# Performance work log

Measured on AMD Instinct MI355X. Metric: run time of the kernel, lower is better.

The kernel has to match this reference:

```python
import jax, jax.numpy as jnp
import numpy as np

B, D, H = 4096, 66, 512  # batch, system dim (22 atoms * 3), MLP hidden


def _dynamics(t, xs, W1, b1, W2, b2, W3, b3):
    # CNF vector field f(t, x): 3-layer SiLU MLP on concat([x, t])
    h = jnp.concatenate([xs, t], axis=1)          # [B, D+1]
    h = jax.nn.silu(h @ W1 + b1)                  # [B, H]
    h = jax.nn.silu(h @ W2 + b2)                  # [B, H]
    return h @ W3 + b3                            # [B, D]


def setup_inputs() -> dict:
    key = jax.random.key(0)
    ks = jax.random.split(key, 5)
    xs = jax.random.normal(ks[0], (B, D), dtype=jnp.float32)
    t = jax.random.uniform(ks[1], (B, 1), dtype=jnp.float32)
    W1 = jax.random.normal(ks[2], (D + 1, H), dtype=jnp.float32) / np.float32(np.sqrt(D + 1))
    b1 = jnp.zeros((H,), dtype=jnp.float32)
    W2 = jax.random.normal(ks[3], (H, H), dtype=jnp.float32) / np.float32(np.sqrt(H))
    b2 = jnp.zeros((H,), dtype=jnp.float32)
    W3 = jax.random.normal(ks[4], (H, D), dtype=jnp.float32) / np.float32(np.sqrt(H))
    b3 = jnp.zeros((D,), dtype=jnp.float32)
    return {"xs": xs, "t": t, "W1": W1, "b1": b1, "W2": W2, "b2": b2, "W3": W3, "b3": b3}


def reference(xs, t, W1, b1, W2, b2, W3, b3):
    # Exact divergence: trace of Jacobian d f / d x, computed with D JVPs
    # (forward-mode equivalent of the torch per-dim autograd.grad loop).
    def f(x):
        return _dynamics(t, x, W1, b1, W2, b2, W3, b3)

    dxs = f(xs)                                   # [B, D]
    eye = jnp.eye(D, dtype=xs.dtype)              # basis vectors e_i

    def jvp_col(e):
        _, tang = jax.jvp(f, (xs,), (jnp.broadcast_to(e, xs.shape),))
        return tang                               # J @ e_i, shape [B, D]

    tangs = jax.vmap(jvp_col)(eye)                # [D, B, D]
    div = jnp.einsum('dbd->b', tangs)             # sum_i (J e_i)_i = tr(J)
    return dxs, -div[:, None]
```

## Files before the change

### kernel.cpp

```cpp
#include <hip/hip_runtime.h>

#define Bn 4096
#define Dn 66
#define Hn 512

typedef __attribute__((ext_vector_type(8))) short short8;
typedef __attribute__((ext_vector_type(4))) float f32x4;

__device__ __forceinline__ unsigned short f2bf(float x) {
    union { float f; unsigned u; } v; v.f = x;
    unsigned r = v.u + 0x7fffu + ((v.u >> 16) & 1u);
    return (unsigned short)(r >> 16);
}
__device__ __forceinline__ float bf2f(unsigned short h) {
    union { float f; unsigned u; } v; v.u = ((unsigned)h) << 16; return v.f;
}


__global__ __launch_bounds__(512, 2) void k_pack(
    const float* __restrict__ W1, const float* __restrict__ W2,
    const float* __restrict__ W3,
    unsigned short* __restrict__ WQ, unsigned short* __restrict__ W3P)
{
    __shared__ float sW3[16*68];
    const int bid = blockIdx.x, tid = threadIdx.x;
    const int lane = tid & 63, wv = tid >> 6;

    if (bid < 64) {
        const int ct = bid >> 1;
        {
            const int r = tid >> 5, ii = tid & 31;
            const float* src = &W3[(size_t)(ct*16 + r)*Dn];
            sW3[r*68 + ii] = src[ii];
            sW3[r*68 + ii + 32] = src[ii + 32];
            if (ii < 2) sW3[r*68 + ii + 64] = src[ii + 64];
        }
        __syncthreads();
        const int ks = (bid & 1)*8 + wv;
        const int n = lane & 15, kg = lane >> 4;
        const int c = ct*16 + n;
        const int abase = ks*32 + kg*8;
        float w2v[8], m[8];
        #pragma unroll
        for (int j = 0; j < 8; ++j) {
            w2v[j] = W2[(size_t)(abase + j)*Hn + c];
            m[j] = 0.f;
        }
        #pragma unroll 2
        for (int i = 0; i < Dn; ++i) {
            const float w3 = sW3[n*68 + i];
            const float4 w1a = *(const float4*)&W1[(size_t)i*Hn + abase];
            const float4 w1b = *(const float4*)&W1[(size_t)i*Hn + abase + 4];
            m[0] = fmaf(w3, w1a.x, m[0]); m[1] = fmaf(w3, w1a.y, m[1]);
            m[2] = fmaf(w3, w1a.z, m[2]); m[3] = fmaf(w3, w1a.w, m[3]);
            m[4] = fmaf(w3, w1b.x, m[4]); m[5] = fmaf(w3, w1b.y, m[5]);
            m[6] = fmaf(w3, w1b.z, m[6]); m[7] = fmaf(w3, w1b.w, m[7]);
        }
        short8 pw, pc;
        #pragma unroll
        for (int j = 0; j < 8; ++j) {
            pw[j] = (short)f2bf(w2v[j]);
            pc[j] = (short)f2bf(w2v[j] * m[j]);
        }
        const size_t off = ((size_t)(ct*16 + ks)*64 + lane)*16;
        *(short8*)&WQ[off]     = pw;
        *(short8*)&WQ[off + 8] = pc;
    } else {
        const int tix = (bid - 64)*8 + wv;
        if (tix < 80) {
            const int ks = tix & 15;
            const int n = lane & 15, kg = lane >> 4;
            const int j_out = (tix >> 4)*16 + n;
            const int abase = ks*32 + kg*8;
            short8 p;
            #pragma unroll
            for (int j = 0; j < 8; ++j)
                p[j] = (j_out < Dn) ? (short)f2bf(W3[(size_t)(abase + j)*Dn + j_out]) : (short)0;
            *(short8*)&W3P[((size_t)tix*64 + lane)*8] = p;
        }
    }
}

__global__ __launch_bounds__(1024, 4) void k_main(
    const float* __restrict__ xs, const float* __restrict__ tt,
    const float* __restrict__ W1, const float* __restrict__ b1,
    const unsigned short* __restrict__ WQ, const float* __restrict__ b2,
    const unsigned short* __restrict__ W3P, const float* __restrict__ b3,
    float* __restrict__ out)
{
    __shared__ __align__(16) unsigned short sA[2*8192];
    __shared__ float sX[67*16];
    __shared__ float sRed[16*16];

    const int tid = threadIdx.x, lane = tid & 63, wv = tid >> 6;
    const int rt = blockIdx.x, r0 = rt*16;
    const int n = lane & 15, kg = lane >> 4;
    const int rot = (blockIdx.x >> 3) & 15;

    for (int idx = tid; idx < 67*16; idx += 1024) {
        const int i = idx >> 4, r = idx & 15;
        sX[idx] = (i < Dn) ? xs[(size_t)(r0+r)*Dn + i] : tt[r0+r];
    }
    __syncthreads();

    {
        const int rg = lane & 7, cg = lane >> 3;
        const int c0 = wv*32 + cg*4;
        const int irot = (blockIdx.x >> 3) & 31;
        float z[2][4];
        {
            const float4 b4 = *(const float4*)&b1[c0];
            z[0][0]=b4.x; z[0][1]=b4.y; z[0][2]=b4.z; z[0][3]=b4.w;
            z[1][0]=b4.x; z[1][1]=b4.y; z[1][2]=b4.z; z[1][3]=b4.w;
        }
        #pragma unroll 2
        for (int s = 0; s < 67; ++s) {
            int i = s + irot; if (i >= 67) i -= 67;
            const float2 xf = *(const float2*)&sX[i*16 + 2*rg];
            const float4 wA = *(const float4*)&W1[(size_t)i*Hn + c0];
            const float ww[4] = {wA.x, wA.y, wA.z, wA.w};
            #pragma unroll
            for (int j = 0; j < 4; ++j) {
                z[0][j] = fmaf(xf.x, ww[j], z[0][j]);
                z[1][j] = fmaf(xf.y, ww[j], z[1][j]);
            }
        }
        const int kgrp = cg >> 1, joff = (cg & 1)*4;
        #pragma unroll
        for (int rr = 0; rr < 2; ++rr) {
            const int r = 2*(lane & 7) + rr;
            ushort4 phi, ps;
            unsigned short* PH = (unsigned short*)&phi;
            unsigned short* PS = (unsigned short*)&ps;
            #pragma unroll
            for (int j = 0; j < 4; ++j) {
                const float zv = z[rr][j];
                const float sg = 1.f / (1.f + __expf(-zv));
                PH[j] = f2bf(zv * sg);
                PS[j] = f2bf(sg * (1.f + zv * (1.f - sg)));
            }
            const int off = (wv*64 + r + 16*kgrp)*8 + joff;
            *(ushort4*)&sA[off]        = phi;
            *(ushort4*)&sA[8192 + off] = ps;
        }
    }
    __syncthreads();

    const int ctb = wv*2;
    f32x4 zac[2], vac[2];
    #pragma unroll
    for (int ti = 0; ti < 2; ++ti) {
        const float bz = b2[(ctb + ti)*16 + n];
        zac[ti] = (f32x4){bz, bz, bz, bz};
        vac[ti] = (f32x4){0.f, 0.f, 0.f, 0.f};
    }
    short8 wbuf[2][2], qbuf[2][2];
    #pragma unroll
    for (int ti = 0; ti < 2; ++ti) {
        const size_t wo = ((size_t)((ctb + ti)*16 + rot)*64 + lane)*16;
        wbuf[0][ti] = *(const short8*)&WQ[wo];
        qbuf[0][ti] = *(const short8*)&WQ[wo + 8];
    }
    #pragma unroll
    for (int s = 0; s < 16; ++s) {
        const int cur = s & 1, nxt = cur ^ 1;
        if (s < 15) {
            const int ksn = (s + 1 + rot) & 15;
            #pragma unroll
            for (int ti = 0; ti < 2; ++ti) {
                const size_t wo = ((size_t)((ctb + ti)*16 + ksn)*64 + lane)*16;
                wbuf[nxt][ti] = *(const short8*)&WQ[wo];
                qbuf[nxt][ti] = *(const short8*)&WQ[wo + 8];
            }
        }
        const int ks = (s + rot) & 15;
        const int ao = (ks*64 + lane)*8;
        const short8 ahi = *(const short8*)&sA[ao];
        const short8 as1 = *(const short8*)&sA[8192 + ao];
        #pragma unroll
        for (int ti = 0; ti < 2; ++ti) {
            zac[ti] = __builtin_amdgcn_mfma_f32_16x16x32_bf16(ahi, wbuf[cur][ti], zac[ti], 0, 0, 0);
            vac[ti] = __builtin_amdgcn_mfma_f32_16x16x32_bf16(as1, qbuf[cur][ti], vac[ti], 0, 0, 0);
        }
    }
    __syncthreads();

    float dp[4] = {0.f, 0.f, 0.f, 0.f};
    #pragma unroll
    for (int ti = 0; ti < 2; ++ti) {
        const int c = (ctb + ti)*16 + n;
        const int ks2 = c >> 5, kg2 = (c >> 3) & 3, j2 = c & 7;
        #pragma unroll
        for (int q = 0; q < 4; ++q) {
            const float z2 = zac[ti][q];
            const float sg = 1.f / (1.f + __expf(-z2));
            const float h2 = z2 * sg;
            dp[q] = fmaf(sg * (1.f + z2 * (1.f - sg)), vac[ti][q], dp[q]);
            const unsigned short hh = f2bf(h2);
            const int o = (ks2*64 + (kg*4 + q) + 16*kg2)*8 + j2;
            sA[o] = hh;
            sA[8192 + o] = f2bf(h2 - bf2f(hh));
        }
    }
    #pragma unroll
    for (int q = 0; q < 4; ++q) {
        float v = dp[q];
        v += __shfl_xor(v, 1, 64);
        v += __shfl_xor(v, 2, 64);
        v += __shfl_xor(v, 4, 64);
        v += __shfl_xor(v, 8, 64);
        if (n == 0) sRed[wv*16 + kg*4 + q] = v;
    }
    __syncthreads();

    if (tid < 16) {
        float s = 0.f;
        #pragma unroll
        for (int q = 0; q < 16; ++q) s += sRed[q*16 + tid];
        out[(size_t)Bn*Dn + r0 + tid] = -s;
    }

    if (wv < 5) {
        const int jt = wv;
        const int j = jt*16 + n;
        const float bj = (j < Dn) ? b3[j] : 0.f;
        f32x4 oac = (f32x4){bj, bj, bj, bj};
        #pragma unroll 4
        for (int s = 0; s < 16; ++s) {
            const int ks = (s + rot) & 15;
            const int aoff = (ks*64 + lane)*8;
            const short8 ahi = *(const short8*)&sA[aoff];
            const short8 alo = *(const short8*)&sA[8192 + aoff];
            const short8 wf  = *(const short8*)&W3P[((size_t)(jt*16 + ks)*64 + lane)*8];
            oac = __builtin_amdgcn_mfma_f32_16x16x32_bf16(ahi, wf, oac, 0, 0, 0);
            oac = __builtin_amdgcn_mfma_f32_16x16x32_bf16(alo, wf, oac, 0, 0, 0);
        }
        if (j < Dn) {
            #pragma unroll
            for (int q = 0; q < 4; ++q)
                out[(size_t)(r0 + kg*4 + q)*Dn + j] = oac[q];
        }
    }
}

extern "C" void kernel_launch(void* const* d_in, const int* in_sizes, int n_in,
                              void* d_out, int out_size, void* d_ws, size_t ws_size,
                              hipStream_t stream)
{
    const float* xs = (const float*)d_in[0];
    const float* t  = (const float*)d_in[1];
    const float* W1 = (const float*)d_in[2];
    const float* b1 = (const float*)d_in[3];
    const float* W2 = (const float*)d_in[4];
    const float* b2 = (const float*)d_in[5];
    const float* W3 = (const float*)d_in[6];
    const float* b3 = (const float*)d_in[7];
    float* out = (float*)d_out;

    char* ws = (char*)d_ws;
    unsigned short* WQ  = (unsigned short*)(ws);
    unsigned short* W3P = (unsigned short*)(ws + 1048576);

    k_pack<<<74,  512,  0, stream>>>(W1, W2, W3, WQ, W3P);
    k_main<<<256, 1024, 0, stream>>>(xs, t, W1, b1, WQ, b2, W3P, b3, out);
}
```

Baseline: 107.8 us.

## Move layer-1 compute into pack kernel and stream h1 operands from global

Layer 1 (x·W1, SiLU, and its derivative) moves out of the main kernel into the pack kernel, which grows to 586 blocks so the row-tile work runs in parallel with weight packing. The main kernel then loads the bf16 h1 and s1 fragments from workspace with double-buffered global loads next to the WQ loads, and no longer needs the LDS staging or the first barriers. This shortens the serial prologue of the main kernel. In exchange, about 8 MB of workspace is written and read back through global memory or L2.

```diff
diff --git a/kernel.cpp b/kernel.cpp
--- a/kernel.cpp
+++ b/kernel.cpp
@@ -17,26 +17,77 @@
 }
 
 
-__global__ __launch_bounds__(512, 2) void k_pack(
-    const float* __restrict__ W1, const float* __restrict__ W2,
-    const float* __restrict__ W3,
-    unsigned short* __restrict__ WQ, unsigned short* __restrict__ W3P)
+__global__ __launch_bounds__(512, 2) void k_h1pack(
+    const float* __restrict__ xs, const float* __restrict__ tt,
+    const float* __restrict__ W1, const float* __restrict__ b1,
+    const float* __restrict__ W2, const float* __restrict__ W3,
+    unsigned short* __restrict__ WQ, unsigned short* __restrict__ W3P,
+    unsigned short* __restrict__ h1hiP, unsigned short* __restrict__ s1P)
 {
-    __shared__ float sW3[16*68];
+    __shared__ float sLds[16*68];
     const int bid = blockIdx.x, tid = threadIdx.x;
     const int lane = tid & 63, wv = tid >> 6;
 
-    if (bid < 64) {
-        const int ct = bid >> 1;
+    if (bid < 512) {
+        const int rt = bid >> 1, half = bid & 1;
+        const int r0 = rt*16;
+        for (int idx = tid; idx < 67*16; idx += 512) {
+            const int i = idx >> 4, r = idx & 15;
+            sLds[idx] = (i < Dn) ? xs[(size_t)(r0+r)*Dn + i] : tt[r0+r];
+        }
+        __syncthreads();
+        const int rg = lane & 7, cg = lane >> 3;
+        const int ks = half*8 + wv;
+        const int c0 = ks*32 + cg*4;
+        const int irot = (bid >> 3) & 31;
+        float z[2][4];
+        {
+            const float4 b4 = *(const float4*)&b1[c0];
+            z[0][0]=b4.x; z[0][1]=b4.y; z[0][2]=b4.z; z[0][3]=b4.w;
+            z[1][0]=b4.x; z[1][1]=b4.y; z[1][2]=b4.z; z[1][3]=b4.w;
+        }
+        #pragma unroll 2
+        for (int s = 0; s < 67; ++s) {
+            int i = s + irot; if (i >= 67) i -= 67;
+            const float2 xf = *(const float2*)&sLds[i*16 + 2*rg];
+            const float4 wA = *(const float4*)&W1[(size_t)i*Hn + c0];
+            const float ww[4] = {wA.x, wA.y, wA.z, wA.w};
+            #pragma unroll
+            for (int j = 0; j < 4; ++j) {
+                z[0][j] = fmaf(xf.x, ww[j], z[0][j]);
+                z[1][j] = fmaf(xf.y, ww[j], z[1][j]);
+            }
+        }
+        const int kgrp = cg >> 1, joff = (cg & 1)*4;
+        #pragma unroll
+        for (int rr = 0; rr < 2; ++rr) {
+            const int r = 2*rg + rr;
+            ushort4 phi, ps;
+            unsigned short* PH = (unsigned short*)&phi;
+            unsigned short* PS = (unsigned short*)&ps;
+            #pragma unroll
+            for (int j = 0; j < 4; ++j) {
+                const float zv = z[rr][j];
+                const float sg = 1.f / (1.f + __expf(-zv));
+                PH[j] = f2bf(zv * sg);
+                PS[j] = f2bf(sg * (1.f + zv * (1.f - sg)));
+            }
+            const size_t off = ((size_t)(rt*16 + ks)*64 + r + 16*kgrp)*8 + joff;
+            *(ushort4*)&h1hiP[off] = phi;
+            *(ushort4*)&s1P [off] = ps;
+        }
+    } else if (bid < 576) {
+        const int pb = bid - 512;
+        const int ct = pb >> 1;
         {
             const int r = tid >> 5, ii = tid & 31;
             const float* src = &W3[(size_t)(ct*16 + r)*Dn];
-            sW3[r*68 + ii] = src[ii];
-            sW3[r*68 + ii + 32] = src[ii + 32];
-            if (ii < 2) sW3[r*68 + ii + 64] = src[ii + 64];
+            sLds[r*68 + ii] = src[ii];
+            sLds[r*68 + ii + 32] = src[ii + 32];
+            if (ii < 2) sLds[r*68 + ii + 64] = src[ii + 64];
         }
         __syncthreads();
-        const int ks = (bid & 1)*8 + wv;
+        const int ks = (pb & 1)*8 + wv;
         const int n = lane & 15, kg = lane >> 4;
         const int c = ct*16 + n;
         const int abase = ks*32 + kg*8;
@@ -48,7 +99,7 @@
         }
         #pragma unroll 2
         for (int i = 0; i < Dn; ++i) {
-            const float w3 = sW3[n*68 + i];
+            const float w3 = sLds[n*68 + i];
             const float4 w1a = *(const float4*)&W1[(size_t)i*Hn + abase];
             const float4 w1b = *(const float4*)&W1[(size_t)i*Hn + abase + 4];
             m[0] = fmaf(w3, w1a.x, m[0]); m[1] = fmaf(w3, w1a.y, m[1]);
@@ -66,7 +117,7 @@
         *(short8*)&WQ[off]     = pw;
         *(short8*)&WQ[off + 8] = pc;
     } else {
-        const int tix = (bid - 64)*8 + wv;
+        const int tix = (bid - 576)*8 + wv;
         if (tix < 80) {
             const int ks = tix & 15;
             const int n = lane & 15, kg = lane >> 4;
@@ -81,15 +132,14 @@
     }
 }
 
-__global__ __launch_bounds__(1024, 4) void k_main(
-    const float* __restrict__ xs, const float* __restrict__ tt,
-    const float* __restrict__ W1, const float* __restrict__ b1,
+__global__ __launch_bounds__(1024, 4) void k_BC(
+    const unsigned short* __restrict__ h1hiP, const unsigned short* __restrict__ s1P,
     const unsigned short* __restrict__ WQ, const float* __restrict__ b2,
     const unsigned short* __restrict__ W3P, const float* __restrict__ b3,
     float* __restrict__ out)
 {
-    __shared__ __align__(16) unsigned short sA[2*8192];
-    __shared__ float sX[67*16];
+    __shared__ __align__(16) unsigned short sH[8192];
+    __shared__ __align__(16) unsigned short sL[8192];
     __shared__ float sRed[16*16];
 
     const int tid = threadIdx.x, lane = tid & 63, wv = tid >> 6;
@@ -97,55 +147,6 @@
     const int n = lane & 15, kg = lane >> 4;
     const int rot = (blockIdx.x >> 3) & 15;
 
-    for (int idx = tid; idx < 67*16; idx += 1024) {
-        const int i = idx >> 4, r = idx & 15;
-        sX[idx] = (i < Dn) ? xs[(size_t)(r0+r)*Dn + i] : tt[r0+r];
-    }
-    __syncthreads();
-
-    {
-        const int rg = lane & 7, cg = lane >> 3;
-        const int c0 = wv*32 + cg*4;
-        const int irot = (blockIdx.x >> 3) & 31;
-        float z[2][4];
-        {
-            const float4 b4 = *(const float4*)&b1[c0];
-            z[0][0]=b4.x; z[0][1]=b4.y; z[0][2]=b4.z; z[0][3]=b4.w;
-            z[1][0]=b4.x; z[1][1]=b4.y; z[1][2]=b4.z; z[1][3]=b4.w;
-        }
-        #pragma unroll 2
-        for (int s = 0; s < 67; ++s) {
-            int i = s + irot; if (i >= 67) i -= 67;
-            const float2 xf = *(const float2*)&sX[i*16 + 2*rg];
-            const float4 wA = *(const float4*)&W1[(size_t)i*Hn + c0];
-            const float ww[4] = {wA.x, wA.y, wA.z, wA.w};
-            #pragma unroll
-            for (int j = 0; j < 4; ++j) {
-                z[0][j] = fmaf(xf.x, ww[j], z[0][j]);
-                z[1][j] = fmaf(xf.y, ww[j], z[1][j]);
-            }
-        }
-        const int kgrp = cg >> 1, joff = (cg & 1)*4;
-        #pragma unroll
-        for (int rr = 0; rr < 2; ++rr) {
-            const int r = 2*(lane & 7) + rr;
-            ushort4 phi, ps;
-            unsigned short* PH = (unsigned short*)&phi;
-            unsigned short* PS = (unsigned short*)&ps;
-            #pragma unroll
-            for (int j = 0; j < 4; ++j) {
-                const float zv = z[rr][j];
-                const float sg = 1.f / (1.f + __expf(-zv));
-                PH[j] = f2bf(zv * sg);
-                PS[j] = f2bf(sg * (1.f + zv * (1.f - sg)));
-            }
-            const int off = (wv*64 + r + 16*kgrp)*8 + joff;
-            *(ushort4*)&sA[off]        = phi;
-            *(ushort4*)&sA[8192 + off] = ps;
-        }
-    }
-    __syncthreads();
-
     const int ctb = wv*2;
     f32x4 zac[2], vac[2];
     #pragma unroll
@@ -154,18 +155,26 @@
         zac[ti] = (f32x4){bz, bz, bz, bz};
         vac[ti] = (f32x4){0.f, 0.f, 0.f, 0.f};
     }
-    short8 wbuf[2][2], qbuf[2][2];
-    #pragma unroll
-    for (int ti = 0; ti < 2; ++ti) {
-        const size_t wo = ((size_t)((ctb + ti)*16 + rot)*64 + lane)*16;
-        wbuf[0][ti] = *(const short8*)&WQ[wo];
-        qbuf[0][ti] = *(const short8*)&WQ[wo + 8];
+    short8 wbuf[2][2], qbuf[2][2], abuf[2], sbuf[2];
+    {
+        const size_t ao = ((size_t)(rt*16 + rot)*64 + lane)*8;
+        abuf[0] = *(const short8*)&h1hiP[ao];
+        sbuf[0] = *(const short8*)&s1P[ao];
+        #pragma unroll
+        for (int ti = 0; ti < 2; ++ti) {
+            const size_t wo = ((size_t)((ctb + ti)*16 + rot)*64 + lane)*16;
+            wbuf[0][ti] = *(const short8*)&WQ[wo];
+            qbuf[0][ti] = *(const short8*)&WQ[wo + 8];
+        }
     }
     #pragma unroll
     for (int s = 0; s < 16; ++s) {
         const int cur = s & 1, nxt = cur ^ 1;
         if (s < 15) {
             const int ksn = (s + 1 + rot) & 15;
+            const size_t ao = ((size_t)(rt*16 + ksn)*64 + lane)*8;
+            abuf[nxt] = *(const short8*)&h1hiP[ao];
+            sbuf[nxt] = *(const short8*)&s1P[ao];
             #pragma unroll
             for (int ti = 0; ti < 2; ++ti) {
                 const size_t wo = ((size_t)((ctb + ti)*16 + ksn)*64 + lane)*16;
@@ -173,17 +182,12 @@
                 qbuf[nxt][ti] = *(const short8*)&WQ[wo + 8];
             }
         }
-        const int ks = (s + rot) & 15;
-        const int ao = (ks*64 + lane)*8;
-        const short8 ahi = *(const short8*)&sA[ao];
-        const short8 as1 = *(const short8*)&sA[8192 + ao];
         #pragma unroll
         for (int ti = 0; ti < 2; ++ti) {
-            zac[ti] = __builtin_amdgcn_mfma_f32_16x16x32_bf16(ahi, wbuf[cur][ti], zac[ti], 0, 0, 0);
-            vac[ti] = __builtin_amdgcn_mfma_f32_16x16x32_bf16(as1, qbuf[cur][ti], vac[ti], 0, 0, 0);
-        }
-    }
-    __syncthreads();
+            zac[ti] = __builtin_amdgcn_mfma_f32_16x16x32_bf16(abuf[cur], wbuf[cur][ti], zac[ti], 0, 0, 0);
+            vac[ti] = __builtin_amdgcn_mfma_f32_16x16x32_bf16(sbuf[cur], qbuf[cur][ti], vac[ti], 0, 0, 0);
+        }
+    }
 
     float dp[4] = {0.f, 0.f, 0.f, 0.f};
     #pragma unroll
@@ -198,8 +202,8 @@
             dp[q] = fmaf(sg * (1.f + z2 * (1.f - sg)), vac[ti][q], dp[q]);
             const unsigned short hh = f2bf(h2);
             const int o = (ks2*64 + (kg*4 + q) + 16*kg2)*8 + j2;
-            sA[o] = hh;
-            sA[8192 + o] = f2bf(h2 - bf2f(hh));
+            sH[o] = hh;
+            sL[o] = f2bf(h2 - bf2f(hh));
         }
     }
     #pragma unroll
@@ -229,8 +233,8 @@
         for (int s = 0; s < 16; ++s) {
             const int ks = (s + rot) & 15;
             const int aoff = (ks*64 + lane)*8;
-            const short8 ahi = *(const short8*)&sA[aoff];
-            const short8 alo = *(const short8*)&sA[8192 + aoff];
+            const short8 ahi = *(const short8*)&sH[aoff];
+            const short8 alo = *(const short8*)&sL[aoff];
             const short8 wf  = *(const short8*)&W3P[((size_t)(jt*16 + ks)*64 + lane)*8];
             oac = __builtin_amdgcn_mfma_f32_16x16x32_bf16(ahi, wf, oac, 0, 0, 0);
             oac = __builtin_amdgcn_mfma_f32_16x16x32_bf16(alo, wf, oac, 0, 0, 0);
@@ -258,9 +262,11 @@
     float* out = (float*)d_out;
 
     char* ws = (char*)d_ws;
-    unsigned short* WQ  = (unsigned short*)(ws);
-    unsigned short* W3P = (unsigned short*)(ws + 1048576);
-
-    k_pack<<<74,  512,  0, stream>>>(W1, W2, W3, WQ, W3P);
-    k_main<<<256, 1024, 0, stream>>>(xs, t, W1, b1, WQ, b2, W3P, b3, out);
-}
+    unsigned short* WQ   = (unsigned short*)(ws);
+    unsigned short* W3P  = (unsigned short*)(ws + 1048576);
+    unsigned short* h1hi = (unsigned short*)(ws + 1130496);
+    unsigned short* s1   = (unsigned short*)(ws + 5324800);
+
+    k_h1pack<<<586, 512,  0, stream>>>(xs, t, W1, b1, W2, W3, WQ, W3P, h1hi, s1);
+    k_BC    <<<256, 1024, 0, stream>>>(h1hi, s1, WQ, b2, W3P, b3, out);
+}
```

Result: no change. 106.3 us (-1.3%).
